# Performance work log

Measured on AMD Instinct MI355X. Metric: run time of the kernel, lower is better.

## Reference

```python
import jax, jax.numpy as jnp
import numpy as np

N_POWER_ITER = 5


def _spectral_normalize(w, n_iter=N_POWER_ITER):
    # w: [out, in] 1x1-conv weight; divide by top singular value (power iteration,
    # deterministic init), mirroring torch.nn.utils.spectral_norm's reparameterization.
    u = jnp.full((w.shape[0],), 1.0 / np.sqrt(w.shape[0]), dtype=w.dtype)
    for _ in range(n_iter):
        v = w.T @ u
        v = v / (jnp.linalg.norm(v) + 1e-12)
        u = w @ v
        u = u / (jnp.linalg.norm(u) + 1e-12)
    sigma = u @ (w @ v)
    return w / sigma


def _maxpool2x2(x):
    # x: [B, C, H, W] -> [B, C, H//2, W//2]
    B, C, H, W = x.shape
    return x.reshape(B, C, H // 2, 2, W // 2, 2).max(axis=(3, 5))


def _conv1x1(w, x):
    # 1x1 conv == channel-mixing einsum. w: [out, in], x: [B, in, H, W]
    return jnp.einsum('oc,bchw->bohw', w, x)


def setup_inputs() -> dict:
    key = jax.random.key(0)
    kx, kq, kk, kv, ko = jax.random.split(key, 5)
    C = 512
    B, H, W = 16, 64, 64
    scale = 0.05
    return {
        'x': jax.random.normal(kx, (B, C, H, W), dtype=jnp.float32),
        'Wq': jax.random.normal(kq, (C // 8, C), dtype=jnp.float32) * scale,
        'Wk': jax.random.normal(kk, (C // 8, C), dtype=jnp.float32) * scale,
        'Wv': jax.random.normal(kv, (C // 2, C), dtype=jnp.float32) * scale,
        'Wo': jax.random.normal(ko, (C, C // 2), dtype=jnp.float32) * scale,
        'gamma': jnp.array([0.5], dtype=jnp.float32),
    }


def reference(x, Wq, Wk, Wv, Wo, gamma):
    B, C, H, W = x.shape
    n_ftrs = H * W
    wq = _spectral_normalize(Wq)
    wk = _spectral_normalize(Wk)
    wv = _spectral_normalize(Wv)
    wo = _spectral_normalize(Wo)
    f = _conv1x1(wq, x).reshape(B, C // 8, n_ftrs)                      # [B, C/8, HW]
    g = _maxpool2x2(_conv1x1(wk, x)).reshape(B, C // 8, n_ftrs // 4)    # [B, C/8, HW/4]
    h = _maxpool2x2(_conv1x1(wv, x)).reshape(B, C // 2, n_ftrs // 4)    # [B, C/2, HW/4]
    # scores: [B, HW, HW/4]; softmax over kv positions
    beta = jax.nn.softmax(jnp.einsum('bcn,bcm->bnm', f, g), axis=-1)
    # attention output: [B, C/2, HW]
    o = jnp.einsum('bcm,bnm->bcn', h, beta).reshape(B, C // 2, H, W)
    o = _conv1x1(wo, o)                                                 # [B, C, H, W]
    return gamma.reshape(()) * o + x
```

## Files before the change

kernel.cpp:

```cpp
#include <hip/hip_runtime.h>
#include <cstdint>

typedef __attribute__((ext_vector_type(8))) short bf16x8;
typedef __attribute__((ext_vector_type(4))) float f32x4;
typedef __attribute__((ext_vector_type(2))) unsigned int u32x2;

#define B_   16
#define C_   512
#define HW_  4096
#define M3_  384
#define HWP_ 1024
#define CV_  256

__device__ __forceinline__ unsigned short f2b(float f) {
  union { float f; unsigned u; } v; v.f = f;
  unsigned r = v.u + 0x7fffu + ((v.u >> 16) & 1u);
  return (unsigned short)(r >> 16);
}
__device__ __forceinline__ float b2f(unsigned short b) {
  union { unsigned u; float f; } v; v.u = ((unsigned)b) << 16;
  return v.f;
}
__device__ __forceinline__ f32x4 mfma16(bf16x8 a, bf16x8 b, f32x4 c) {
  return __builtin_amdgcn_mfma_f32_16x16x32_bf16(a, b, c, 0, 0, 0);
}

__global__ __launch_bounds__(256) void k_transpose(const float* __restrict__ x,
                                                   unsigned short* __restrict__ xb) {
  __shared__ unsigned short t[64][66];
  const int b = blockIdx.z, k0 = blockIdx.y * 64, n0 = blockIdx.x * 64;
  const float* xp = x + (size_t)b * C_ * HW_;
  const int ln = threadIdx.x & 63, g = threadIdx.x >> 6;
  for (int kk = g; kk < 64; kk += 4)
    t[kk][ln] = f2b(xp[(size_t)(k0 + kk) * HW_ + n0 + ln]);
  __syncthreads();
  unsigned short* xo = xb + (size_t)b * HW_ * C_;
  for (int nn = g; nn < 64; nn += 4)
    xo[(size_t)(n0 + nn) * C_ + k0 + ln] = t[ln][nn];
}

__global__ __launch_bounds__(256) void k_wtrans(
    const float* __restrict__ Wq, const float* __restrict__ Wk,
    const float* __restrict__ Wv, const float* __restrict__ Wo,
    float* __restrict__ wt) {
  const float* w; int out, in; float* dst;
  switch (blockIdx.z) {
    case 0: w = Wq; out = 64;  in = 512; dst = wt;          break;
    case 1: w = Wk; out = 64;  in = 512; dst = wt + 32768;  break;
    case 2: w = Wv; out = 256; in = 512; dst = wt + 65536;  break;
    default: w = Wo; out = 512; in = 256; dst = wt + 196608; break;
  }
  const int o0 = blockIdx.y * 64, i0 = blockIdx.x * 64;
  if (o0 >= out || i0 >= in) return;
  __shared__ float t[64][65];
  const int ln = threadIdx.x & 63, g = threadIdx.x >> 6;
  for (int oo = g; oo < 64; oo += 4)
    t[oo][ln] = w[(size_t)(o0 + oo) * in + i0 + ln];
  __syncthreads();
  for (int ii = g; ii < 64; ii += 4)
    dst[(size_t)(i0 + ii) * out + o0 + ln] = t[ln][ii];
}

__device__ __forceinline__ float breduce1024(float val, float* red) {
  __syncthreads();
#pragma unroll
  for (int off = 32; off > 0; off >>= 1) val += __shfl_down(val, off);
  if ((threadIdx.x & 63) == 0) red[threadIdx.x >> 6] = val;
  __syncthreads();
  float s = 0.f;
#pragma unroll
  for (int i = 0; i < 16; ++i) s += red[i];
  return s;
}

__global__ __launch_bounds__(1024) void k_specnorm(
    const float* __restrict__ Wq, const float* __restrict__ Wk,
    const float* __restrict__ Wv, const float* __restrict__ Wo,
    const float* __restrict__ wt,
    unsigned short* __restrict__ wqkv, unsigned short* __restrict__ wob) {
  __shared__ float u[512], v[512];
  __shared__ float part[4096];
  __shared__ float red[16];
  const float* w; const float* wT; int out, in; unsigned short* dst;
  switch (blockIdx.x) {
    case 0: w = Wq; wT = wt;          out = 64;  in = 512; dst = wqkv;             break;
    case 1: w = Wk; wT = wt + 32768;  out = 64;  in = 512; dst = wqkv + 64 * 512;  break;
    case 2: w = Wv; wT = wt + 65536;  out = 256; in = 512; dst = wqkv + 128 * 512; break;
    default: w = Wo; wT = wt + 196608; out = 512; in = 256; dst = wob;             break;
  }
  const int tid = threadIdx.x;
  const float rs = rsqrtf((float)out);
  if (tid < out) u[tid] = rs;
  __syncthreads();
  for (int it = 0; it < 5; ++it) {
    {
      const int G = in >> 2, nch = 1024 / G;
      const int ch = tid / G, grp = tid - ch * G;
      const int rpc = out / nch, obase = ch * rpc;
      f32x4 acc = {0.f, 0.f, 0.f, 0.f};
#pragma unroll 8
      for (int r = 0; r < rpc; ++r) {
        const int o = obase + r;
        const f32x4 wv = *reinterpret_cast<const f32x4*>(&w[(size_t)o * in + grp * 4]);
        const float uo = u[o];
        acc[0] += wv[0] * uo; acc[1] += wv[1] * uo;
        acc[2] += wv[2] * uo; acc[3] += wv[3] * uo;
      }
      *reinterpret_cast<f32x4*>(&part[ch * in + grp * 4]) = acc;
      __syncthreads();
      if (tid < in) {
        float s = 0.f;
        for (int c2 = 0; c2 < nch; ++c2) s += part[c2 * in + tid];
        v[tid] = s;
      }
    }
    {
      float ss = 0.f;
      __syncthreads();
      if (tid < in) ss = v[tid] * v[tid];
      ss = breduce1024(ss, red);
      const float sv = 1.f / (sqrtf(ss) + 1e-12f);
      if (tid < in) v[tid] *= sv;
      __syncthreads();
    }
    {
      const int G = out >> 2, nch = 1024 / G;
      const int ch = tid / G, grp = tid - ch * G;
      const int cpc = in / nch, cbase = ch * cpc;
      f32x4 acc = {0.f, 0.f, 0.f, 0.f};
#pragma unroll 8
      for (int r = 0; r < cpc; ++r) {
        const int c = cbase + r;
        const f32x4 wv = *reinterpret_cast<const f32x4*>(&wT[(size_t)c * out + grp * 4]);
        const float vc = v[c];
        acc[0] += wv[0] * vc; acc[1] += wv[1] * vc;
        acc[2] += wv[2] * vc; acc[3] += wv[3] * vc;
      }
      *reinterpret_cast<f32x4*>(&part[ch * out + grp * 4]) = acc;
      __syncthreads();
      if (tid < out) {
        float s = 0.f;
        for (int c2 = 0; c2 < nch; ++c2) s += part[c2 * out + tid];
        u[tid] = s;
      }
    }
    {
      float su = 0.f;
      __syncthreads();
      if (tid < out) su = u[tid] * u[tid];
      su = breduce1024(su, red);
      const float sv2 = 1.f / (sqrtf(su) + 1e-12f);
      if (tid < out) u[tid] *= sv2;
      __syncthreads();
    }
  }
  float sp = 0.f;
  {
    const int G = out >> 2, nch = 1024 / G;
    const int ch = tid / G, grp = tid - ch * G;
    const int cpc = in / nch, cbase = ch * cpc;
    f32x4 acc = {0.f, 0.f, 0.f, 0.f};
#pragma unroll 8
    for (int r = 0; r < cpc; ++r) {
      const int c = cbase + r;
      const f32x4 wv = *reinterpret_cast<const f32x4*>(&wT[(size_t)c * out + grp * 4]);
      const float vc = v[c];
      acc[0] += wv[0] * vc; acc[1] += wv[1] * vc;
      acc[2] += wv[2] * vc; acc[3] += wv[3] * vc;
    }
    *reinterpret_cast<f32x4*>(&part[ch * out + grp * 4]) = acc;
    __syncthreads();
    if (tid < out) {
      float s = 0.f;
      for (int c2 = 0; c2 < nch; ++c2) s += part[c2 * out + tid];
      sp = s * u[tid];
    }
  }
  sp = breduce1024(sp, red);
  const float oscale = (blockIdx.x == 0) ? 1.44269504f : 1.0f;
  const float inv_sigma = (1.f / sp) * oscale;
  const int total = out * in;
  for (int i = tid * 4; i < total; i += 4096) {
    const f32x4 wv = *reinterpret_cast<const f32x4*>(&w[i]);
    u32x2 pw;
    pw[0] = ((unsigned)f2b(wv[1] * inv_sigma) << 16) | f2b(wv[0] * inv_sigma);
    pw[1] = ((unsigned)f2b(wv[3] * inv_sigma) << 16) | f2b(wv[2] * inv_sigma);
    *reinterpret_cast<u32x2*>(&dst[i]) = pw;
  }
}

__global__ __launch_bounds__(256) void k_gemm_qkv(
    const unsigned short* __restrict__ xb, const unsigned short* __restrict__ wqkv,
    unsigned short* __restrict__ yt) {
  __shared__ alignas(16) char smem[32768];
  unsigned short* As = (unsigned short*)smem;
  unsigned short* Bs = (unsigned short*)(smem + 16384);
  const int lid = blockIdx.x;
  const int swz = (lid & 7) * 192 + (lid >> 3);
  const int mt = swz % 3, rest = swz / 3;
  const int nt = rest & 31, b = rest >> 5;
  const int n0 = nt * 128, m0 = mt * 128;
  const unsigned short* Ap = xb + (size_t)b * HW_ * C_ + (size_t)n0 * C_;
  const unsigned short* Bp = wqkv + (size_t)m0 * C_;
  const int tid = threadIdx.x, lane = tid & 63, wid = tid >> 6;
  const int wn = (wid >> 1) * 64, wm = (wid & 1) * 64;
  f32x4 acc[4][4] = {};
  for (int k0 = 0; k0 < C_; k0 += 64) {
    __syncthreads();
#pragma unroll
    for (int i = 0; i < 4; ++i) {
      const int r = i * 32 + (tid >> 3);
      const int s = tid & 7, ss = s ^ (r & 7);
      *reinterpret_cast<f32x4*>(&As[r * 64 + ss * 8]) =
          *reinterpret_cast<const f32x4*>(&Ap[(size_t)r * C_ + k0 + s * 8]);
      *reinterpret_cast<f32x4*>(&Bs[r * 64 + ss * 8]) =
          *reinterpret_cast<const f32x4*>(&Bp[(size_t)r * C_ + k0 + s * 8]);
    }
    __syncthreads();
#pragma unroll
    for (int kk = 0; kk < 2; ++kk) {
      bf16x8 af[4], bfr[4];
#pragma unroll
      for (int i = 0; i < 4; ++i) {
        const int r = wn + i * 16 + (lane & 15);
        const int slot = (kk * 4 + (lane >> 4)) ^ (r & 7);
        af[i] = *reinterpret_cast<const bf16x8*>(&As[r * 64 + slot * 8]);
      }
#pragma unroll
      for (int j = 0; j < 4; ++j) {
        const int r = wm + j * 16 + (lane & 15);
        const int slot = (kk * 4 + (lane >> 4)) ^ (r & 7);
        bfr[j] = *reinterpret_cast<const bf16x8*>(&Bs[r * 64 + slot * 8]);
      }
#pragma unroll
      for (int i = 0; i < 4; ++i)
#pragma unroll
        for (int j = 0; j < 4; ++j) acc[i][j] = mfma16(af[i], bfr[j], acc[i][j]);
    }
  }
  unsigned short* eps = (unsigned short*)smem;
  unsigned short* Y = yt + (size_t)b * HW_ * M3_;
#pragma unroll
  for (int h = 0; h < 2; ++h) {
    __syncthreads();
    if ((wid >> 1) == h) {
#pragma unroll
      for (int i = 0; i < 4; ++i)
#pragma unroll
        for (int j = 0; j < 4; ++j)
#pragma unroll
          for (int r = 0; r < 4; ++r) {
            const int nl = i * 16 + (lane >> 4) * 4 + r;
            const int ml = wm + j * 16 + (lane & 15);
            eps[nl * 136 + ml] = f2b(acc[i][j][r]);
          }
    }
    __syncthreads();
#pragma unroll
    for (int t = 0; t < 4; ++t) {
      const int row = t * 16 + (tid >> 4);
      const int m8 = (tid & 15) * 8;
      *reinterpret_cast<f32x4*>(&Y[(size_t)(n0 + h * 64 + row) * M3_ + m0 + m8]) =
          *reinterpret_cast<const f32x4*>(&eps[row * 136 + m8]);
    }
  }
}

__global__ __launch_bounds__(256) void k_pool_g(const unsigned short* __restrict__ yt,
                                                unsigned short* __restrict__ gt) {
  const int b = blockIdx.y, mp0 = blockIdx.x * 64;
  const int c = threadIdx.x & 63, dm = threadIdx.x >> 6;
  const unsigned short* Y = yt + (size_t)b * HW_ * M3_;
  unsigned short* G = gt + (size_t)b * HWP_ * 64;
  for (int mm = dm; mm < 64; mm += 4) {
    const int mp = mp0 + mm;
    const int n00 = (mp >> 5) * 128 + (mp & 31) * 2;
    const float a0 = b2f(Y[(size_t)n00 * M3_ + 64 + c]);
    const float a1 = b2f(Y[(size_t)(n00 + 1) * M3_ + 64 + c]);
    const float a2 = b2f(Y[(size_t)(n00 + 64) * M3_ + 64 + c]);
    const float a3 = b2f(Y[(size_t)(n00 + 65) * M3_ + 64 + c]);
    G[(size_t)mp * 64 + c] = f2b(fmaxf(fmaxf(a0, a1), fmaxf(a2, a3)));
  }
}

__global__ __launch_bounds__(256) void k_pool_vt(const unsigned short* __restrict__ yt,
                                                 unsigned short* __restrict__ vt) {
  __shared__ unsigned short t[64][66];
  const int b = blockIdx.z, mp0 = blockIdx.x * 64, cv0 = blockIdx.y * 64;
  const unsigned short* Y = yt + (size_t)b * HW_ * M3_;
  const int c = threadIdx.x & 63, dm = threadIdx.x >> 6;
  for (int mm = dm; mm < 64; mm += 4) {
    const int mp = mp0 + mm;
    const int n00 = (mp >> 5) * 128 + (mp & 31) * 2;
    const float a0 = b2f(Y[(size_t)n00 * M3_ + 128 + cv0 + c]);
    const float a1 = b2f(Y[(size_t)(n00 + 1) * M3_ + 128 + cv0 + c]);
    const float a2 = b2f(Y[(size_t)(n00 + 64) * M3_ + 128 + cv0 + c]);
    const float a3 = b2f(Y[(size_t)(n00 + 65) * M3_ + 128 + cv0 + c]);
    t[mm][c] = f2b(fmaxf(fmaxf(a0, a1), fmaxf(a2, a3)));
  }
  __syncthreads();
  unsigned short* V = vt + (size_t)b * CV_ * HWP_;
  for (int cc = dm; cc < 64; cc += 4)
    V[(size_t)(cv0 + cc) * HWP_ + mp0 + c] = t[c][cc];
}

__global__ __launch_bounds__(256, 2) void k_attn(
    const unsigned short* __restrict__ yt, const unsigned short* __restrict__ gt,
    const unsigned short* __restrict__ vt, unsigned short* __restrict__ oat) {
  __shared__ alignas(16) char smem[49152];
  const int lid = blockIdx.x;
  const int swz = (lid & 7) * 64 + (lid >> 3);
  const int q0 = (swz & 31) * 128, b = swz >> 5;
  const int tid = threadIdx.x, lane = tid & 63, wid = tid >> 6;
  const int q = lane & 15, g = lane >> 4;
  const unsigned short* Qg = yt + (size_t)b * HW_ * M3_ + (size_t)(q0 + wid * 32) * M3_;
  const unsigned short* Gg = gt + (size_t)b * HWP_ * 64;
  const unsigned short* Vg = vt + (size_t)b * CV_ * HWP_;
  unsigned short* P = (unsigned short*)(smem + 40960) + wid * 1024;
  bf16x8 qf[2][2];
#pragma unroll
  for (int h = 0; h < 2; ++h)
#pragma unroll
    for (int kk = 0; kk < 2; ++kk)
      qf[h][kk] = *reinterpret_cast<const bf16x8*>(&Qg[(size_t)(h * 16 + q) * M3_ + kk * 32 + g * 8]);
  const int kr = tid >> 3, ks = tid & 7;
  f32x4 kreg, vreg[4];
  kreg = *reinterpret_cast<const f32x4*>(&Gg[(size_t)kr * 64 + ks * 8]);
#pragma unroll
  for (int t = 0; t < 4; ++t) {
    const int i = tid + t * 256, r = i >> 2, s = i & 3;
    vreg[t] = *reinterpret_cast<const f32x4*>(&Vg[(size_t)r * HWP_ + s * 8]);
  }
  {
    unsigned short* Kb = (unsigned short*)smem;
    unsigned short* Vb = (unsigned short*)(smem + 8192);
    *reinterpret_cast<f32x4*>(&Kb[kr * 64 + (ks ^ (kr & 7)) * 8]) = kreg;
#pragma unroll
    for (int t = 0; t < 4; ++t) {
      const int i = tid + t * 256, r = i >> 2, s = i & 3;
      *reinterpret_cast<f32x4*>(&Vb[r * 32 + (s ^ (r & 3)) * 8]) = vreg[t];
    }
  }
  kreg = *reinterpret_cast<const f32x4*>(&Gg[(size_t)(32 + kr) * 64 + ks * 8]);
#pragma unroll
  for (int t = 0; t < 4; ++t) {
    const int i = tid + t * 256, r = i >> 2, s = i & 3;
    vreg[t] = *reinterpret_cast<const f32x4*>(&Vg[(size_t)r * HWP_ + 32 + s * 8]);
  }
  __syncthreads();
  f32x4 oacc[2][16] = {};
  float m_run[2] = {-1e30f, -1e30f}, l_run[2] = {0.f, 0.f};
  for (int it = 0; it < 32; ++it) {
    const int cur = it & 1;
    unsigned short* Kc = (unsigned short*)(smem + cur * 4096);
    unsigned short* Vc = (unsigned short*)(smem + 8192 + cur * 16384);
    if (it < 31) {
      unsigned short* Kn = (unsigned short*)(smem + (cur ^ 1) * 4096);
      unsigned short* Vn = (unsigned short*)(smem + 8192 + (cur ^ 1) * 16384);
      *reinterpret_cast<f32x4*>(&Kn[kr * 64 + (ks ^ (kr & 7)) * 8]) = kreg;
#pragma unroll
      for (int t = 0; t < 4; ++t) {
        const int i = tid + t * 256, r = i >> 2, s = i & 3;
        *reinterpret_cast<f32x4*>(&Vn[r * 32 + (s ^ (r & 3)) * 8]) = vreg[t];
      }
    }
    if (it < 30) {
      const int kvn = (it + 2) * 32;
      kreg = *reinterpret_cast<const f32x4*>(&Gg[(size_t)(kvn + kr) * 64 + ks * 8]);
#pragma unroll
      for (int t = 0; t < 4; ++t) {
        const int i = tid + t * 256, r = i >> 2, s = i & 3;
        vreg[t] = *reinterpret_cast<const f32x4*>(&Vg[(size_t)r * HWP_ + kvn + s * 8]);
      }
    }
    f32x4 sacc[2][2] = {};
#pragma unroll
    for (int kk = 0; kk < 2; ++kk) {
      bf16x8 kf[2];
#pragma unroll
      for (int i = 0; i < 2; ++i) {
        const int row = i * 16 + q;
        const int sl = (kk * 4 + g) ^ (row & 7);
        kf[i] = *reinterpret_cast<const bf16x8*>(&Kc[row * 64 + sl * 8]);
      }
#pragma unroll
      for (int h = 0; h < 2; ++h)
#pragma unroll
        for (int i = 0; i < 2; ++i) sacc[h][i] = mfma16(kf[i], qf[h][kk], sacc[h][i]);
    }
#pragma unroll
    for (int h = 0; h < 2; ++h) {
      float tmax = -1e30f;
#pragma unroll
      for (int i = 0; i < 2; ++i)
#pragma unroll
        for (int r = 0; r < 4; ++r) tmax = fmaxf(tmax, sacc[h][i][r]);
      tmax = fmaxf(tmax, __shfl_xor(tmax, 16));
      tmax = fmaxf(tmax, __shfl_xor(tmax, 32));
      if (__any(tmax > m_run[h] + 11.0f)) {
        const float mnew = fmaxf(m_run[h], tmax);
        const float alpha = exp2f(m_run[h] - mnew);
        m_run[h] = mnew;
        l_run[h] *= alpha;
        float al[4];
#pragma unroll
        for (int r = 0; r < 4; ++r) al[r] = __shfl(alpha, g * 4 + r);
#pragma unroll
        for (int j = 0; j < 16; ++j) {
          oacc[h][j][0] *= al[0]; oacc[h][j][1] *= al[1];
          oacc[h][j][2] *= al[2]; oacc[h][j][3] *= al[3];
        }
      }
      const int qg = h * 16 + q;
      float lsum = 0.f;
#pragma unroll
      for (int i = 0; i < 2; ++i) {
        const float p0 = exp2f(sacc[h][i][0] - m_run[h]);
        const float p1 = exp2f(sacc[h][i][1] - m_run[h]);
        const float p2 = exp2f(sacc[h][i][2] - m_run[h]);
        const float p3 = exp2f(sacc[h][i][3] - m_run[h]);
        lsum += (p0 + p1) + (p2 + p3);
        u32x2 pw;
        pw[0] = ((unsigned)f2b(p1) << 16) | f2b(p0);
        pw[1] = ((unsigned)f2b(p3) << 16) | f2b(p2);
        const int c = 2 * i + (g >> 1);
        *reinterpret_cast<u32x2*>(&P[qg * 32 + ((c ^ (qg & 3)) * 8) + (g & 1) * 4]) = pw;
      }
      lsum += __shfl_xor(lsum, 16);
      lsum += __shfl_xor(lsum, 32);
      l_run[h] += lsum;
    }
    __builtin_amdgcn_s_setprio(1);
    bf16x8 pa[2];
#pragma unroll
    for (int h = 0; h < 2; ++h) {
      const int qg = h * 16 + q;
      pa[h] = *reinterpret_cast<const bf16x8*>(&P[qg * 32 + ((g ^ (qg & 3)) * 8)]);
    }
#pragma unroll
    for (int j = 0; j < 16; ++j) {
      const int row = j * 16 + q;
      const int sl = g ^ (row & 3);
      const bf16x8 vf = *reinterpret_cast<const bf16x8*>(&Vc[row * 32 + sl * 8]);
      oacc[0][j] = mfma16(pa[0], vf, oacc[0][j]);
      oacc[1][j] = mfma16(pa[1], vf, oacc[1][j]);
    }
    __builtin_amdgcn_s_setprio(0);
    __syncthreads();
  }
  float linv[2][4];
#pragma unroll
  for (int h = 0; h < 2; ++h) {
    const float myinv = 1.f / l_run[h];
#pragma unroll
    for (int r = 0; r < 4; ++r) linv[h][r] = __shfl(myinv, g * 4 + r);
  }
  unsigned short* eps = (unsigned short*)smem;
  unsigned short* O = oat + (size_t)b * HW_ * CV_ + (size_t)q0 * CV_;
#pragma unroll
  for (int ch = 0; ch < 2; ++ch) {
    __syncthreads();
    if ((wid >> 1) == ch) {
#pragma unroll
      for (int h = 0; h < 2; ++h)
#pragma unroll
        for (int j = 0; j < 16; ++j)
#pragma unroll
          for (int r = 0; r < 4; ++r) {
            const int row = (wid & 1) * 32 + h * 16 + g * 4 + r;
            const int cv = j * 16 + q;
            eps[row * 264 + cv] = f2b(oacc[h][j][r] * linv[h][r]);
          }
    }
    __syncthreads();
#pragma unroll
    for (int t = 0; t < 8; ++t) {
      const int row = t * 8 + (tid >> 5);
      const int cv8 = (tid & 31) * 8;
      *reinterpret_cast<f32x4*>(&O[(size_t)(ch * 64 + row) * CV_ + cv8]) =
          *reinterpret_cast<const f32x4*>(&eps[row * 264 + cv8]);
    }
  }
}

__global__ __launch_bounds__(256) void k_gemm_out(
    const unsigned short* __restrict__ oat, const unsigned short* __restrict__ wob,
    const float* __restrict__ x, const float* __restrict__ gamma,
    float* __restrict__ out) {
  __shared__ alignas(16) char smem[32768];
  unsigned short* As = (unsigned short*)smem;
  unsigned short* Bs = (unsigned short*)(smem + 16384);
  const int lid = blockIdx.x;
  const int swz = (lid & 7) * 256 + (lid >> 3);
  const int ct = swz & 3, nt = (swz >> 2) & 31, b = swz >> 7;
  const int n0 = nt * 128, co0 = ct * 128;
  const unsigned short* Ap = wob + (size_t)co0 * CV_;
  const unsigned short* Bp = oat + (size_t)b * HW_ * CV_ + (size_t)n0 * CV_;
  const int tid = threadIdx.x, lane = tid & 63, wid = tid >> 6;
  const int wc = (wid >> 1) * 64, wn = (wid & 1) * 64;
  f32x4 acc[4][4] = {};
  for (int k0 = 0; k0 < CV_; k0 += 64) {
    __syncthreads();
#pragma unroll
    for (int i = 0; i < 4; ++i) {
      const int r = i * 32 + (tid >> 3);
      const int s = tid & 7, ss = s ^ (r & 7);
      *reinterpret_cast<f32x4*>(&As[r * 64 + ss * 8]) =
          *reinterpret_cast<const f32x4*>(&Ap[(size_t)r * CV_ + k0 + s * 8]);
      *reinterpret_cast<f32x4*>(&Bs[r * 64 + ss * 8]) =
          *reinterpret_cast<const f32x4*>(&Bp[(size_t)r * CV_ + k0 + s * 8]);
    }
    __syncthreads();
#pragma unroll
    for (int kk = 0; kk < 2; ++kk) {
      bf16x8 af[4], bfr[4];
#pragma unroll
      for (int i = 0; i < 4; ++i) {
        const int r = wc + i * 16 + (lane & 15);
        const int slot = (kk * 4 + (lane >> 4)) ^ (r & 7);
        af[i] = *reinterpret_cast<const bf16x8*>(&As[r * 64 + slot * 8]);
      }
#pragma unroll
      for (int j = 0; j < 4; ++j) {
        const int r = wn + j * 16 + (lane & 15);
        const int slot = (kk * 4 + (lane >> 4)) ^ (r & 7);
        bfr[j] = *reinterpret_cast<const bf16x8*>(&Bs[r * 64 + slot * 8]);
      }
#pragma unroll
      for (int i = 0; i < 4; ++i)
#pragma unroll
        for (int j = 0; j < 4; ++j) acc[i][j] = mfma16(af[i], bfr[j], acc[i][j]);
    }
  }
  float* eps = (float*)smem;
  const float g = gamma[0];
  const size_t base = (size_t)b * C_ * HW_;
#pragma unroll
  for (int h = 0; h < 4; ++h) {
    __syncthreads();
    if ((wid >> 1) == (h >> 1)) {
#pragma unroll
      for (int ii = 0; ii < 2; ++ii) {
        const int i = (h & 1) * 2 + ii;
#pragma unroll
        for (int j = 0; j < 4; ++j)
#pragma unroll
          for (int r = 0; r < 4; ++r) {
            const int col2 = ii * 16 + (lane >> 4) * 4 + r;
            const int nl = wn + j * 16 + (lane & 15);
            eps[col2 * 132 + nl] = acc[i][j][r];
          }
      }
    }
    __syncthreads();
#pragma unroll
    for (int t = 0; t < 4; ++t) {
      const int row = t * 8 + (tid >> 5);
      const int col = (tid & 31) * 4;
      const size_t goff = base + (size_t)(co0 + h * 32 + row) * HW_ + n0 + col;
      const f32x4 xv = *reinterpret_cast<const f32x4*>(&x[goff]);
      const f32x4 av = *reinterpret_cast<const f32x4*>(&eps[row * 132 + col]);
      f32x4 ov;
      ov[0] = g * av[0] + xv[0];
      ov[1] = g * av[1] + xv[1];
      ov[2] = g * av[2] + xv[2];
      ov[3] = g * av[3] + xv[3];
      *reinterpret_cast<f32x4*>(&out[goff]) = ov;
    }
  }
}

extern "C" void kernel_launch(void* const* d_in, const int* in_sizes, int n_in,
                              void* d_out, int out_size, void* d_ws, size_t ws_size,
                              hipStream_t stream) {
  (void)in_sizes; (void)n_in; (void)out_size; (void)ws_size;
  const float* x     = (const float*)d_in[0];
  const float* Wq    = (const float*)d_in[1];
  const float* Wk    = (const float*)d_in[2];
  const float* Wv    = (const float*)d_in[3];
  const float* Wo    = (const float*)d_in[4];
  const float* gamma = (const float*)d_in[5];
  float* out = (float*)d_out;
  char* ws = (char*)d_ws;

  unsigned short* wqkv = (unsigned short*)(ws);
  unsigned short* wob  = (unsigned short*)(ws + 393216);
  unsigned short* xb   = (unsigned short*)(ws + 655360);
  unsigned short* yt   = (unsigned short*)(ws + 67764224);
  unsigned short* gt   = (unsigned short*)(ws + 118095872);
  unsigned short* vt   = (unsigned short*)(ws + 120193024);
  unsigned short* oat  = xb;
  float* wt = (float*)yt;

  k_transpose<<<dim3(64, 8, 16), 256, 0, stream>>>(x, xb);
  k_wtrans<<<dim3(8, 8, 4), 256, 0, stream>>>(Wq, Wk, Wv, Wo, wt);
  k_specnorm<<<4, 1024, 0, stream>>>(Wq, Wk, Wv, Wo, wt, wqkv, wob);
  k_gemm_qkv<<<1536, 256, 0, stream>>>(xb, wqkv, yt);
  k_pool_g<<<dim3(16, 16), 256, 0, stream>>>(yt, gt);
  k_pool_vt<<<dim3(16, 4, 16), 256, 0, stream>>>(yt, vt);
  k_attn<<<512, 256, 0, stream>>>(yt, gt, vt, oat);
  k_gemm_out<<<2048, 256, 0, stream>>>(oat, wob, x, gamma, out);
}
```

Before: 296.3 us.

## Use direct global-to-LDS loads in GEMMs and pad attention LDS tiles

In the QKV projection and output projection GEMMs, the register-staged global→LDS copies become global_load_lds 16-byte direct loads. The XOR swizzle moves to the global source address so the LDS layout stays compatible with the existing reads. In the attention kernel, the XOR-swizzled V and P shared-memory layouts become padded rows (stride 40 instead of 32), which raises LDS use to about 58KB per block. The aim is to drop VGPR round trips and index math, at the risk of bank conflicts or reduced occupancy from the larger LDS footprint.

```diff
diff --git a/kernel.cpp b/kernel.cpp
--- a/kernel.cpp
+++ b/kernel.cpp
@@ -23,6 +23,11 @@
 }
 __device__ __forceinline__ f32x4 mfma16(bf16x8 a, bf16x8 b, f32x4 c) {
   return __builtin_amdgcn_mfma_f32_16x16x32_bf16(a, b, c, 0, 0, 0);
+}
+__device__ __forceinline__ void gload_lds16(const unsigned short* g, unsigned short* l) {
+  __builtin_amdgcn_global_load_lds(
+      (const __attribute__((address_space(1))) void*)g,
+      (__attribute__((address_space(3))) void*)l, 16, 0, 0);
 }
 
 __global__ __launch_bounds__(256) void k_transpose(const float* __restrict__ x,
@@ -210,11 +215,11 @@
 #pragma unroll
     for (int i = 0; i < 4; ++i) {
       const int r = i * 32 + (tid >> 3);
-      const int s = tid & 7, ss = s ^ (r & 7);
-      *reinterpret_cast<f32x4*>(&As[r * 64 + ss * 8]) =
-          *reinterpret_cast<const f32x4*>(&Ap[(size_t)r * C_ + k0 + s * 8]);
-      *reinterpret_cast<f32x4*>(&Bs[r * 64 + ss * 8]) =
-          *reinterpret_cast<const f32x4*>(&Bp[(size_t)r * C_ + k0 + s * 8]);
+      const int s = tid & 7;
+      const int rw = i * 32 + wid * 8;
+      const size_t goff = (size_t)r * C_ + k0 + (size_t)((s ^ (r & 7)) * 8);
+      gload_lds16(&Ap[goff], &As[rw * 64]);
+      gload_lds16(&Bp[goff], &Bs[rw * 64]);
     }
     __syncthreads();
 #pragma unroll
@@ -307,7 +312,7 @@
 __global__ __launch_bounds__(256, 2) void k_attn(
     const unsigned short* __restrict__ yt, const unsigned short* __restrict__ gt,
     const unsigned short* __restrict__ vt, unsigned short* __restrict__ oat) {
-  __shared__ alignas(16) char smem[49152];
+  __shared__ alignas(16) char smem[59392];
   const int lid = blockIdx.x;
   const int swz = (lid & 7) * 64 + (lid >> 3);
   const int q0 = (swz & 31) * 128, b = swz >> 5;
@@ -316,7 +321,7 @@
   const unsigned short* Qg = yt + (size_t)b * HW_ * M3_ + (size_t)(q0 + wid * 32) * M3_;
   const unsigned short* Gg = gt + (size_t)b * HWP_ * 64;
   const unsigned short* Vg = vt + (size_t)b * CV_ * HWP_;
-  unsigned short* P = (unsigned short*)(smem + 40960) + wid * 1024;
+  unsigned short* P = (unsigned short*)(smem + 49152) + wid * 1280;
   bf16x8 qf[2][2];
 #pragma unroll
   for (int h = 0; h < 2; ++h)
@@ -338,7 +343,7 @@
 #pragma unroll
     for (int t = 0; t < 4; ++t) {
       const int i = tid + t * 256, r = i >> 2, s = i & 3;
-      *reinterpret_cast<f32x4*>(&Vb[r * 32 + (s ^ (r & 3)) * 8]) = vreg[t];
+      *reinterpret_cast<f32x4*>(&Vb[r * 40 + s * 8]) = vreg[t];
     }
   }
   kreg = *reinterpret_cast<const f32x4*>(&Gg[(size_t)(32 + kr) * 64 + ks * 8]);
@@ -353,15 +358,15 @@
   for (int it = 0; it < 32; ++it) {
     const int cur = it & 1;
     unsigned short* Kc = (unsigned short*)(smem + cur * 4096);
-    unsigned short* Vc = (unsigned short*)(smem + 8192 + cur * 16384);
+    unsigned short* Vc = (unsigned short*)(smem + 8192 + cur * 20480);
     if (it < 31) {
       unsigned short* Kn = (unsigned short*)(smem + (cur ^ 1) * 4096);
-      unsigned short* Vn = (unsigned short*)(smem + 8192 + (cur ^ 1) * 16384);
+      unsigned short* Vn = (unsigned short*)(smem + 8192 + (cur ^ 1) * 20480);
       *reinterpret_cast<f32x4*>(&Kn[kr * 64 + (ks ^ (kr & 7)) * 8]) = kreg;
 #pragma unroll
       for (int t = 0; t < 4; ++t) {
         const int i = tid + t * 256, r = i >> 2, s = i & 3;
-        *reinterpret_cast<f32x4*>(&Vn[r * 32 + (s ^ (r & 3)) * 8]) = vreg[t];
+        *reinterpret_cast<f32x4*>(&Vn[r * 40 + s * 8]) = vreg[t];
       }
     }
     if (it < 30) {
@@ -424,7 +429,7 @@
         pw[0] = ((unsigned)f2b(p1) << 16) | f2b(p0);
         pw[1] = ((unsigned)f2b(p3) << 16) | f2b(p2);
         const int c = 2 * i + (g >> 1);
-        *reinterpret_cast<u32x2*>(&P[qg * 32 + ((c ^ (qg & 3)) * 8) + (g & 1) * 4]) = pw;
+        *reinterpret_cast<u32x2*>(&P[qg * 40 + c * 8 + (g & 1) * 4]) = pw;
       }
       lsum += __shfl_xor(lsum, 16);
       lsum += __shfl_xor(lsum, 32);
@@ -435,13 +440,12 @@
 #pragma unroll
     for (int h = 0; h < 2; ++h) {
       const int qg = h * 16 + q;
-      pa[h] = *reinterpret_cast<const bf16x8*>(&P[qg * 32 + ((g ^ (qg & 3)) * 8)]);
+      pa[h] = *reinterpret_cast<const bf16x8*>(&P[qg * 40 + g * 8]);
     }
 #pragma unroll
     for (int j = 0; j < 16; ++j) {
       const int row = j * 16 + q;
-      const int sl = g ^ (row & 3);
-      const bf16x8 vf = *reinterpret_cast<const bf16x8*>(&Vc[row * 32 + sl * 8]);
+      const bf16x8 vf = *reinterpret_cast<const bf16x8*>(&Vc[row * 40 + g * 8]);
       oacc[0][j] = mfma16(pa[0], vf, oacc[0][j]);
       oacc[1][j] = mfma16(pa[1], vf, oacc[1][j]);
     }
@@ -504,11 +508,11 @@
 #pragma unroll
     for (int i = 0; i < 4; ++i) {
       const int r = i * 32 + (tid >> 3);
-      const int s = tid & 7, ss = s ^ (r & 7);
-      *reinterpret_cast<f32x4*>(&As[r * 64 + ss * 8]) =
-          *reinterpret_cast<const f32x4*>(&Ap[(size_t)r * CV_ + k0 + s * 8]);
-      *reinterpret_cast<f32x4*>(&Bs[r * 64 + ss * 8]) =
-          *reinterpret_cast<const f32x4*>(&Bp[(size_t)r * CV_ + k0 + s * 8]);
+      const int s = tid & 7;
+      const int rw = i * 32 + wid * 8;
+      const size_t goff = (size_t)r * CV_ + k0 + (size_t)((s ^ (r & 7)) * 8);
+      gload_lds16(&Ap[goff], &As[rw * 64]);
+      gload_lds16(&Bp[goff], &Bs[rw * 64]);
     }
     __syncthreads();
 #pragma unroll
```

After: 292.2 us. No clear change (-1.4%).
